# Kernel tuning notes

Measured on AMD Instinct MI355X. Metric: run time of the kernel, lower is better.

Reference implementation:

```python
import jax, jax.numpy as jnp
import numpy as np

B, N, C, F = 64, 64, 8, 256      # batch, neighbors per sample, in_channels, in_features
OC, OF = 8, 256                  # out_channels, out_features


def setup_inputs() -> dict:
    key = jax.random.key(0)
    k0, k1, k2, k3, k4 = jax.random.split(key, 5)
    x = jax.random.normal(k0, (B, C, F), dtype=jnp.float32)
    neighbor = jax.random.normal(k1, (B, N, C, F), dtype=jnp.float32)
    # att1/att2: nn.Linear(in_features, in_channels, bias=False) -> weight (C, F)
    W1 = jax.random.normal(k2, (C, F), dtype=jnp.float32) * (1.0 / np.sqrt(F))
    W2 = jax.random.normal(k3, (C, F), dtype=jnp.float32) * (1.0 / np.sqrt(F))
    # conv: nn.Conv1d(C, OC*OF, kernel_size=F, bias=False) -> weight (OC*OF, C, F)
    Wc = jax.random.normal(k4, (OC * OF, C, F), dtype=jnp.float32) * (1.0 / np.sqrt(C * F))
    return {"x": x, "neighbor": neighbor, "W1": W1, "W2": W2, "Wc": Wc}


def _sgnroot(a):
    return jnp.sign(a) * jnp.sqrt(jnp.clip(jnp.abs(a), 1e-8))


def _row_normalize(a):
    # torch: x / (x.abs().sum(1, keepdim=True) + 1e-7); dim 1 is the channel dim of (B,C,F,F)
    a = a / (jnp.abs(a).sum(axis=1, keepdims=True) + 1e-7)
    return jnp.where(jnp.isnan(a), 0.0, a)


def _feature_adjacency(x, neighbor, W1, W2):
    # w[b,n] = sum_{c,k} (x[b] @ W1^T)[c,k] * sum_{k,l} (neighbor[b,n] @ W2^T)[k,l]
    s1 = jnp.einsum('bcf,kf->b', x, W1)            # total sum of att1(x[b])
    s2 = jnp.einsum('bncf,kf->bn', neighbor, W2)   # total sum of att2(y[b,n])
    w = s1[:, None] * s2                            # (B, N)
    # fadj[b,c,a,d] = sum_n x[b,c,a] * neighbor[b,n,c,d] * w[b,n]
    fadj = jnp.einsum('bca,bncd,bn->bcad', x, neighbor, w)
    fadj = fadj + jnp.swapaxes(fadj, -2, -1)
    return _row_normalize(_sgnroot(fadj))


def _conv_transform(z, Wc, lead_shape):
    # Conv1d(C, OC*OF, kernel_size=F, bias=False) over (.., C, F) == full contraction
    out = jnp.einsum('...cf,ocf->...o', z, Wc)
    return out.reshape(*lead_shape, OC, OF)


def reference(x, neighbor, W1, W2, Wc):
    adj = _feature_adjacency(x, neighbor, W1, W2)              # (B,C,F,F)
    # transform(x, adj): (adj @ x.unsqueeze(-1)).squeeze(-1) then conv
    zx = jnp.einsum('bcad,bcd->bca', adj, x)                   # (B,C,F)
    x_out = _conv_transform(zx, Wc, (x.shape[0],))             # (B,OC,OF)
    # transform(neighbor[i], adj[i:i+1]) for each i -> adj broadcasts over N
    zn = jnp.einsum('bcad,bncd->bnca', adj, neighbor)          # (B,N,C,F)
    n_out = _conv_transform(zn, Wc, (x.shape[0], neighbor.shape[1]))  # (B,N,OC,OF)
    return x_out, n_out
```

## Files before the change

kernel.cpp:

```cpp
#include <hip/hip_runtime.h>
#include <hip/hip_bf16.h>
#include <math.h>

#define B_ 64
#define N_ 64
#define C_ 8
#define F_ 256
#define K_ 2048
#define NO_ 2048
#define M_TOT 4160

typedef __attribute__((ext_vector_type(8))) short bf16x8;
typedef __attribute__((ext_vector_type(4))) float f32x4;

__global__ __launch_bounds__(256) void sums_k(const float* __restrict__ x,
        const float* __restrict__ nb, const float* __restrict__ W1,
        const float* __restrict__ W2, float* __restrict__ s1,
        float* __restrict__ s2) {
    int blk = blockIdx.x;
    int f = threadIdx.x;
    float val;
    if (blk < B_ * N_) {
        const float* base = nb + (size_t)blk * (C_ * F_);
        float wsum = 0.f;
        #pragma unroll
        for (int k = 0; k < C_; ++k) wsum += W2[k * F_ + f];
        float cs = 0.f;
        #pragma unroll
        for (int c = 0; c < C_; ++c) cs += base[c * F_ + f];
        val = cs * wsum;
    } else {
        int b = blk - B_ * N_;
        const float* base = x + (size_t)b * (C_ * F_);
        float wsum = 0.f;
        #pragma unroll
        for (int k = 0; k < C_; ++k) wsum += W1[k * F_ + f];
        float cs = 0.f;
        #pragma unroll
        for (int c = 0; c < C_; ++c) cs += base[c * F_ + f];
        val = cs * wsum;
    }
    #pragma unroll
    for (int off = 32; off > 0; off >>= 1) val += __shfl_down(val, off, 64);
    __shared__ float wred[4];
    int w = f >> 6;
    if ((f & 63) == 0) wred[w] = val;
    __syncthreads();
    if (f == 0) {
        float s = wred[0] + wred[1] + wred[2] + wred[3];
        if (blk < B_ * N_) s2[blk] = s;
        else s1[blk - B_ * N_] = s;
    }
}

__global__ __launch_bounds__(1024) void t_k(const float* __restrict__ nb,
        const float* __restrict__ s1, const float* __restrict__ s2,
        float* __restrict__ t) {
    int blk = blockIdx.x;
    int b = blk / C_, c = blk % C_;
    int tid = threadIdx.x;
    int q = tid >> 8, d = tid & 255;
    const float* p = nb + ((size_t)(b * N_) * C_ + c) * F_ + d;
    const float* s2p = s2 + b * N_;
    float acc = 0.f;
    #pragma unroll
    for (int j = 0; j < 16; ++j) {
        int n = q * 16 + j;
        acc += p[(size_t)n * C_ * F_] * s2p[n];
    }
    __shared__ float part[4][F_];
    part[q][d] = acc;
    __syncthreads();
    if (tid < 256) {
        float s = part[0][d] + part[1][d] + part[2][d] + part[3][d];
        t[(size_t)blk * F_ + d] = s * s1[b];
    }
}

__global__ __launch_bounds__(256) void denom_k(const float* __restrict__ x,
        const float* __restrict__ t, float* __restrict__ rdenom) {
    int blk = blockIdx.x;
    int b = blk >> 8, a = blk & 255;
    int d = threadIdx.x;
    float acc = 1e-7f;
    #pragma unroll
    for (int c = 0; c < C_; ++c) {
        size_t o = ((size_t)b * C_ + c) * F_;
        float xa = x[o + a], ta = t[o + a];
        float xd = x[o + d], td = t[o + d];
        float v = xa * td + xd * ta;
        float r = __builtin_amdgcn_sqrtf(fmaxf(fabsf(v), 1e-8f));
        acc += (v != 0.f) ? r : 0.f;
    }
    rdenom[(size_t)blk * F_ + d] = __builtin_amdgcn_rcpf(acc);
}

__device__ __forceinline__ float sgnroot_dev(float v) {
    float r = __builtin_amdgcn_sqrtf(fmaxf(fabsf(v), 1e-8f));
    return (v > 0.f) ? r : ((v < 0.f) ? -r : 0.f);
}

__global__ __launch_bounds__(256) void wc_cvt_k(const float* __restrict__ Wc,
        __hip_bfloat16* __restrict__ Bbuf) {
    int i = (blockIdx.x * 256 + threadIdx.x) * 4;
    float4 v = *(const float4*)(Wc + i);
    Bbuf[i + 0] = __float2bfloat16(v.x);
    Bbuf[i + 1] = __float2bfloat16(v.y);
    Bbuf[i + 2] = __float2bfloat16(v.z);
    Bbuf[i + 3] = __float2bfloat16(v.w);
}

#define ZNX_PAD 264
__global__ __launch_bounds__(256) void znx_k(const float* __restrict__ x,
        const float* __restrict__ t, const float* __restrict__ rdenom,
        const float* __restrict__ nb, __hip_bfloat16* __restrict__ Abuf) {
    int bc = blockIdx.x;
    int b = bc >> 3, c = bc & 7;
    int tid = threadIdx.x;
    int wave = tid >> 6, lane = tid & 63;
    __shared__ float xs[F_], ts[F_];
    __shared__ __hip_bfloat16 nbB[80 * ZNX_PAD];

    xs[tid] = x[(size_t)bc * F_ + tid];
    ts[tid] = t[(size_t)bc * F_ + tid];
    {
        int r = tid >> 2, cs0 = (tid & 3) * 64;
        const float* src = nb + (((size_t)(b * N_ + r)) * C_ + c) * F_ + cs0;
        __hip_bfloat16* dst = nbB + r * ZNX_PAD + cs0;
        #pragma unroll
        for (int j = 0; j < 64; j += 4) {
            float4 v = *(const float4*)(src + j);
            dst[j + 0] = __float2bfloat16(v.x);
            dst[j + 1] = __float2bfloat16(v.y);
            dst[j + 2] = __float2bfloat16(v.z);
            dst[j + 3] = __float2bfloat16(v.w);
        }
    }
    if (tid < 64) {
        float4 v = *(const float4*)(x + (size_t)bc * F_ + tid * 4);
        __hip_bfloat16* dst = nbB + 64 * ZNX_PAD + tid * 4;
        dst[0] = __float2bfloat16(v.x);
        dst[1] = __float2bfloat16(v.y);
        dst[2] = __float2bfloat16(v.z);
        dst[3] = __float2bfloat16(v.w);
    }
    {
        __hip_bfloat16 z = __float2bfloat16(0.f);
        #pragma unroll
        for (int j = 0; j < 16; ++j) {
            int o = 65 * ZNX_PAD + tid * 16 + j;
            if (o < 80 * ZNX_PAD) nbB[o] = z;
        }
    }
    __syncthreads();

    const int aq = lane & 15;
    const int dq = lane >> 4;
    #pragma unroll
    for (int atile = 0; atile < 4; ++atile) {
        int a = wave * 64 + atile * 16 + aq;
        float xa = xs[a], ta = ts[a];
        const float* drow = rdenom + ((size_t)b * F_ + a) * F_;
        f32x4 acc[5] = {};
        #pragma unroll
        for (int kc = 0; kc < 8; ++kc) {
            int d0 = kc * 32 + dq * 8;
            float4 xv0 = *(const float4*)(xs + d0);
            float4 xv1 = *(const float4*)(xs + d0 + 4);
            float4 tv0 = *(const float4*)(ts + d0);
            float4 tv1 = *(const float4*)(ts + d0 + 4);
            float4 dn0 = *(const float4*)(drow + d0);
            float4 dn1 = *(const float4*)(drow + d0 + 4);
            float xv[8] = {xv0.x, xv0.y, xv0.z, xv0.w, xv1.x, xv1.y, xv1.z, xv1.w};
            float tv[8] = {tv0.x, tv0.y, tv0.z, tv0.w, tv1.x, tv1.y, tv1.z, tv1.w};
            float dn[8] = {dn0.x, dn0.y, dn0.z, dn0.w, dn1.x, dn1.y, dn1.z, dn1.w};
            union { bf16x8 v; __hip_bfloat16 h[8]; } bu;
            #pragma unroll
            for (int j = 0; j < 8; ++j) {
                float g = sgnroot_dev(xa * tv[j] + xv[j] * ta);
                bu.h[j] = __float2bfloat16(g * dn[j]);
            }
            #pragma unroll
            for (int mt = 0; mt < 5; ++mt) {
                bf16x8 af = *(const bf16x8*)(nbB + (mt * 16 + aq) * ZNX_PAD
                                             + kc * 32 + dq * 8);
                acc[mt] = __builtin_amdgcn_mfma_f32_16x16x32_bf16(
                    af, bu.v, acc[mt], 0, 0, 0);
            }
        }
        int colA = c * F_ + a;
        #pragma unroll
        for (int mt = 0; mt < 4; ++mt) {
            int row = 64 + b * N_ + mt * 16 + dq * 4;
            #pragma unroll
            for (int i = 0; i < 4; ++i)
                Abuf[(size_t)(row + i) * K_ + colA] = __float2bfloat16(acc[mt][i]);
        }
        if (dq == 0)
            Abuf[(size_t)b * K_ + colA] = __float2bfloat16(acc[4][0]);
    }
}

__global__ __launch_bounds__(256) void gemm_bf16_k(
        const __hip_bfloat16* __restrict__ A,
        const __hip_bfloat16* __restrict__ Bm,
        float* __restrict__ Cm) {
    __shared__ char ldsA[128 * 32 * 2] __attribute__((aligned(16)));
    __shared__ char ldsB[128 * 32 * 2] __attribute__((aligned(16)));
    const int t = threadIdx.x;
    const int wave = t >> 6;
    const int lane = t & 63;
    const int col0 = blockIdx.x * 128;
    const int row0 = blockIdx.y * 128;
    const int wrow0 = (wave & 1) * 64;
    const int wcol0 = (wave >> 1) * 64;

    const int rA0 = t >> 2;
    const int kc = (t & 3) * 8;
    const int grA0 = min(row0 + rA0, M_TOT - 1);
    const int grA1 = min(row0 + rA0 + 64, M_TOT - 1);
    const int gcB0 = col0 + rA0;
    const int gcB1 = col0 + rA0 + 64;
    const char* ldsA_u0 = ldsA + ((t >> 6) << 6) * 16;
    const char* ldsA_u1 = ldsA + 4096 + ((t >> 6) << 6) * 16;
    const char* ldsB_u0 = ldsB + ((t >> 6) << 6) * 16;
    const char* ldsB_u1 = ldsB + 4096 + ((t >> 6) << 6) * 16;

    f32x4 acc[4][4] = {};

    for (int k0 = 0; k0 < K_; k0 += 32) {
        __syncthreads();
        __builtin_amdgcn_global_load_lds(
            (const __attribute__((address_space(1))) void*)(A + (size_t)grA0 * K_ + k0 + kc),
            (__attribute__((address_space(3))) void*)ldsA_u0, 16, 0, 0);
        __builtin_amdgcn_global_load_lds(
            (const __attribute__((address_space(1))) void*)(A + (size_t)grA1 * K_ + k0 + kc),
            (__attribute__((address_space(3))) void*)ldsA_u1, 16, 0, 0);
        __builtin_amdgcn_global_load_lds(
            (const __attribute__((address_space(1))) void*)(Bm + (size_t)gcB0 * K_ + k0 + kc),
            (__attribute__((address_space(3))) void*)ldsB_u0, 16, 0, 0);
        __builtin_amdgcn_global_load_lds(
            (const __attribute__((address_space(1))) void*)(Bm + (size_t)gcB1 * K_ + k0 + kc),
            (__attribute__((address_space(3))) void*)ldsB_u1, 16, 0, 0);
        __syncthreads();

        bf16x8 af[4], bf[4];
        #pragma unroll
        for (int rb = 0; rb < 4; ++rb) {
            int off = (wrow0 + rb * 16 + (lane & 15)) * 64 + (lane >> 4) * 16;
            af[rb] = *(const bf16x8*)(ldsA + off);
        }
        #pragma unroll
        for (int cb = 0; cb < 4; ++cb) {
            int off = (wcol0 + cb * 16 + (lane & 15)) * 64 + (lane >> 4) * 16;
            bf[cb] = *(const bf16x8*)(ldsB + off);
        }
        #pragma unroll
        for (int rb = 0; rb < 4; ++rb)
            #pragma unroll
            for (int cb = 0; cb < 4; ++cb)
                acc[rb][cb] = __builtin_amdgcn_mfma_f32_16x16x32_bf16(
                    af[rb], bf[cb], acc[rb][cb], 0, 0, 0);
    }

    #pragma unroll
    for (int rb = 0; rb < 4; ++rb) {
        int rowbase = row0 + wrow0 + rb * 16 + (lane >> 4) * 4;
        #pragma unroll
        for (int cb = 0; cb < 4; ++cb) {
            int col = col0 + wcol0 + cb * 16 + (lane & 15);
            #pragma unroll
            for (int i = 0; i < 4; ++i) {
                int row = rowbase + i;
                if (row < M_TOT)
                    Cm[(size_t)row * NO_ + col] = acc[rb][cb][i];
            }
        }
    }
}

extern "C" void kernel_launch(void* const* d_in, const int* in_sizes, int n_in,
                              void* d_out, int out_size, void* d_ws, size_t ws_size,
                              hipStream_t stream) {
    const float* x  = (const float*)d_in[0];
    const float* nb = (const float*)d_in[1];
    const float* W1 = (const float*)d_in[2];
    const float* W2 = (const float*)d_in[3];
    const float* Wc = (const float*)d_in[4];
    float* out = (float*)d_out;
    float* ws = (float*)d_ws;

    float* s1    = ws;
    float* s2    = ws + 64;
    float* t     = ws + 4160;
    float* rden  = ws + 135232;
    __hip_bfloat16* Abuf = (__hip_bfloat16*)(ws + 4329536);
    __hip_bfloat16* Bbuf = Abuf + (size_t)M_TOT * K_;

    hipLaunchKernelGGL(sums_k, dim3(B_ * N_ + B_), dim3(256), 0, stream,
                       x, nb, W1, W2, s1, s2);
    hipLaunchKernelGGL(t_k, dim3(B_ * C_), dim3(1024), 0, stream, nb, s1, s2, t);
    hipLaunchKernelGGL(denom_k, dim3(B_ * F_), dim3(256), 0, stream, x, t, rden);
    hipLaunchKernelGGL(wc_cvt_k, dim3((K_ * NO_) / 1024), dim3(256), 0, stream,
                       Wc, Bbuf);
    hipLaunchKernelGGL(znx_k, dim3(B_ * C_), dim3(256), 0, stream,
                       x, t, rden, nb, Abuf);
    hipLaunchKernelGGL(gemm_bf16_k, dim3(16, 33), dim3(256), 0, stream,
                       Abuf, Bbuf, out);
}
```

Before: 238.8 us.

## Fuse Wc bf16 conversion into sums kernel and re-layout GEMM LDS tiles

The standalone Wc-to-bf16 conversion kernel is folded into the sums kernel as extra blocks, removing one launch and letting the conversion run alongside the reductions. The GEMM's global-to-LDS staging is reorganised so each wave loads 64 rows of one 8-element k-slab, and LDS is laid out k-slab-major with 16-byte rows. This aims to make the fragment reads conflict-free and the loads contiguous per wave. Each lane now reads 16 bytes per row with a 4 KB stride between its two loads, which may coalesce less well from global memory.

```diff
diff --git a/kernel.cpp b/kernel.cpp
--- a/kernel.cpp
+++ b/kernel.cpp
@@ -13,12 +13,22 @@
 typedef __attribute__((ext_vector_type(8))) short bf16x8;
 typedef __attribute__((ext_vector_type(4))) float f32x4;
 
-__global__ __launch_bounds__(256) void sums_k(const float* __restrict__ x,
+__global__ __launch_bounds__(256) void sums_wc_k(const float* __restrict__ x,
         const float* __restrict__ nb, const float* __restrict__ W1,
-        const float* __restrict__ W2, float* __restrict__ s1,
-        float* __restrict__ s2) {
+        const float* __restrict__ W2, const float* __restrict__ Wc,
+        float* __restrict__ s1, float* __restrict__ s2,
+        __hip_bfloat16* __restrict__ Bbuf) {
     int blk = blockIdx.x;
     int f = threadIdx.x;
+    if (blk >= B_ * N_ + B_) {
+        int i = (blk - (B_ * N_ + B_)) * 1024 + f * 4;
+        float4 v = *(const float4*)(Wc + i);
+        Bbuf[i + 0] = __float2bfloat16(v.x);
+        Bbuf[i + 1] = __float2bfloat16(v.y);
+        Bbuf[i + 2] = __float2bfloat16(v.z);
+        Bbuf[i + 3] = __float2bfloat16(v.w);
+        return;
+    }
     float val;
     if (blk < B_ * N_) {
         const float* base = nb + (size_t)blk * (C_ * F_);
@@ -98,16 +108,6 @@
 __device__ __forceinline__ float sgnroot_dev(float v) {
     float r = __builtin_amdgcn_sqrtf(fmaxf(fabsf(v), 1e-8f));
     return (v > 0.f) ? r : ((v < 0.f) ? -r : 0.f);
-}
-
-__global__ __launch_bounds__(256) void wc_cvt_k(const float* __restrict__ Wc,
-        __hip_bfloat16* __restrict__ Bbuf) {
-    int i = (blockIdx.x * 256 + threadIdx.x) * 4;
-    float4 v = *(const float4*)(Wc + i);
-    Bbuf[i + 0] = __float2bfloat16(v.x);
-    Bbuf[i + 1] = __float2bfloat16(v.y);
-    Bbuf[i + 2] = __float2bfloat16(v.z);
-    Bbuf[i + 3] = __float2bfloat16(v.w);
 }
 
 #define ZNX_PAD 264
@@ -205,8 +205,8 @@
         const __hip_bfloat16* __restrict__ A,
         const __hip_bfloat16* __restrict__ Bm,
         float* __restrict__ Cm) {
-    __shared__ char ldsA[128 * 32 * 2] __attribute__((aligned(16)));
-    __shared__ char ldsB[128 * 32 * 2] __attribute__((aligned(16)));
+    __shared__ char ldsA[8192] __attribute__((aligned(16)));
+    __shared__ char ldsB[8192] __attribute__((aligned(16)));
     const int t = threadIdx.x;
     const int wave = t >> 6;
     const int lane = t & 63;
@@ -214,47 +214,47 @@
     const int row0 = blockIdx.y * 128;
     const int wrow0 = (wave & 1) * 64;
     const int wcol0 = (wave >> 1) * 64;
-
-    const int rA0 = t >> 2;
-    const int kc = (t & 3) * 8;
-    const int grA0 = min(row0 + rA0, M_TOT - 1);
-    const int grA1 = min(row0 + rA0 + 64, M_TOT - 1);
-    const int gcB0 = col0 + rA0;
-    const int gcB1 = col0 + rA0 + 64;
-    const char* ldsA_u0 = ldsA + ((t >> 6) << 6) * 16;
-    const char* ldsA_u1 = ldsA + 4096 + ((t >> 6) << 6) * 16;
-    const char* ldsB_u0 = ldsB + ((t >> 6) << 6) * 16;
-    const char* ldsB_u1 = ldsB + 4096 + ((t >> 6) << 6) * 16;
+    const int aq = lane & 15;
+    const int dq = lane >> 4;
+
+    const int srow = (wave & 1) * 64 + lane;
+    const int slab = wave >> 1;
+    const int grA = min(row0 + srow, M_TOT - 1);
+    const int gcB = col0 + srow;
+    const __hip_bfloat16* gA = A + (size_t)grA * K_ + slab * 8;
+    const __hip_bfloat16* gB = Bm + (size_t)gcB * K_ + slab * 8;
+    char* lA0 = ldsA + wave * 1024;
+    char* lA1 = ldsA + 4096 + wave * 1024;
+    char* lB0 = ldsB + wave * 1024;
+    char* lB1 = ldsB + 4096 + wave * 1024;
 
     f32x4 acc[4][4] = {};
 
     for (int k0 = 0; k0 < K_; k0 += 32) {
         __syncthreads();
         __builtin_amdgcn_global_load_lds(
-            (const __attribute__((address_space(1))) void*)(A + (size_t)grA0 * K_ + k0 + kc),
-            (__attribute__((address_space(3))) void*)ldsA_u0, 16, 0, 0);
+            (const __attribute__((address_space(1))) void*)(gA + k0),
+            (__attribute__((address_space(3))) void*)lA0, 16, 0, 0);
         __builtin_amdgcn_global_load_lds(
-            (const __attribute__((address_space(1))) void*)(A + (size_t)grA1 * K_ + k0 + kc),
-            (__attribute__((address_space(3))) void*)ldsA_u1, 16, 0, 0);
+            (const __attribute__((address_space(1))) void*)(gA + k0 + 16),
+            (__attribute__((address_space(3))) void*)lA1, 16, 0, 0);
         __builtin_amdgcn_global_load_lds(
-            (const __attribute__((address_space(1))) void*)(Bm + (size_t)gcB0 * K_ + k0 + kc),
-            (__attribute__((address_space(3))) void*)ldsB_u0, 16, 0, 0);
+            (const __attribute__((address_space(1))) void*)(gB + k0),
+            (__attribute__((address_space(3))) void*)lB0, 16, 0, 0);
         __builtin_amdgcn_global_load_lds(
-            (const __attribute__((address_space(1))) void*)(Bm + (size_t)gcB1 * K_ + k0 + kc),
-            (__attribute__((address_space(3))) void*)ldsB_u1, 16, 0, 0);
+            (const __attribute__((address_space(1))) void*)(gB + k0 + 16),
+            (__attribute__((address_space(3))) void*)lB1, 16, 0, 0);
         __syncthreads();
 
         bf16x8 af[4], bf[4];
         #pragma unroll
-        for (int rb = 0; rb < 4; ++rb) {
-            int off = (wrow0 + rb * 16 + (lane & 15)) * 64 + (lane >> 4) * 16;
-            af[rb] = *(const bf16x8*)(ldsA + off);
-        }
-        #pragma unroll
-        for (int cb = 0; cb < 4; ++cb) {
-            int off = (wcol0 + cb * 16 + (lane & 15)) * 64 + (lane >> 4) * 16;
-            bf[cb] = *(const bf16x8*)(ldsB + off);
-        }
+        for (int rb = 0; rb < 4; ++rb)
+            af[rb] = *(const bf16x8*)(ldsA + dq * 2048
+                                      + (wrow0 + rb * 16 + aq) * 16);
+        #pragma unroll
+        for (int cb = 0; cb < 4; ++cb)
+            bf[cb] = *(const bf16x8*)(ldsB + dq * 2048
+                                      + (wcol0 + cb * 16 + aq) * 16);
         #pragma unroll
         for (int rb = 0; rb < 4; ++rb)
             #pragma unroll
@@ -297,12 +297,10 @@
     __hip_bfloat16* Abuf = (__hip_bfloat16*)(ws + 4329536);
     __hip_bfloat16* Bbuf = Abuf + (size_t)M_TOT * K_;
 
-    hipLaunchKernelGGL(sums_k, dim3(B_ * N_ + B_), dim3(256), 0, stream,
-                       x, nb, W1, W2, s1, s2);
+    hipLaunchKernelGGL(sums_wc_k, dim3(B_ * N_ + B_ + (K_ * NO_) / 1024),
+                       dim3(256), 0, stream, x, nb, W1, W2, Wc, s1, s2, Bbuf);
     hipLaunchKernelGGL(t_k, dim3(B_ * C_), dim3(1024), 0, stream, nb, s1, s2, t);
     hipLaunchKernelGGL(denom_k, dim3(B_ * F_), dim3(256), 0, stream, x, t, rden);
-    hipLaunchKernelGGL(wc_cvt_k, dim3((K_ * NO_) / 1024), dim3(256), 0, stream,
-                       Wc, Bbuf);
     hipLaunchKernelGGL(znx_k, dim3(B_ * C_), dim3(256), 0, stream,
                        x, t, rden, nb, Abuf);
     hipLaunchKernelGGL(gemm_bf16_k, dim3(16, 33), dim3(256), 0, stream,
```

Measured after the change: 272.6 us. +14.1%, slower.
